# Optimization experiments

Hardware: AMD Instinct MI355X
Metric: run time of the kernel (lower is better)

The kernel has to match this reference:

```python
import jax, jax.numpy as jnp
import numpy as np

B, S, E = 32, 720, 862
PRED_LEN = S
FREQ_TOPK = 20
WINDOW = 24  # fixed optimal_window (code fallback/default candidate)
EPS_VAR = 1e-5


def _main_freq_part(x, k):
    # x: [B, S, E]; rfft over time axis
    xf = jnp.fft.rfft(x, axis=1)                      # [B, F, E] complex
    F = xf.shape[1]
    mag = jnp.moveaxis(jnp.abs(xf), 1, 2)             # [B, E, F]
    _, idx = jax.lax.top_k(mag, k)                    # [B, E, k]
    mask = jnp.sum(jax.nn.one_hot(idx, F, dtype=x.dtype), axis=2)  # [B, E, F]
    mask = jnp.moveaxis(mask, 2, 1)                   # [B, F, E]
    x_filtered = jnp.fft.irfft(xf * mask, axis=1).astype(jnp.float32)  # S even -> length S
    return x - x_filtered, x_filtered


def _window_stats(x, w):
    # Sliding-window mean/std (biased var) with replicate padding, via cumsum.
    pad = w // 2
    xp = jnp.pad(x, ((0, 0), (pad, pad), (0, 0)), mode='edge')  # [B, S+w, E]
    z = jnp.zeros_like(xp[:, :1])
    cs = jnp.concatenate([z, jnp.cumsum(xp, axis=1)], axis=1)
    cs2 = jnp.concatenate([z, jnp.cumsum(xp * xp, axis=1)], axis=1)
    s = x.shape[1]
    s1 = cs[:, w:w + s] - cs[:, :s]
    s2 = cs2[:, w:w + s] - cs2[:, :s]
    mean = s1 / w
    var = jnp.maximum(s2 / w - mean * mean, 0.0)
    std = jnp.sqrt(var + EPS_VAR)
    return mean, std


def _mlp_freq(main_freq_T, x_T, Wf1, bf1, Wf2, bf2, Wf3, bf3):
    # main_freq_T, x_T: [B, E, S]
    h = jax.nn.relu(main_freq_T @ Wf1 + bf1)          # [B, E, 64]
    inp = jnp.concatenate([h, x_T], axis=-1)          # [B, E, 64+S]
    h2 = jax.nn.relu(inp @ Wf2 + bf2)                 # [B, E, 128]
    return h2 @ Wf3 + bf3                             # [B, E, pred_len]


def _mlp_pred(stat_T, x_T, Wp1, bp1, Wp2, bp2, Wp3, bp3):
    h = jax.nn.relu(stat_T @ Wp1 + bp1)               # [B, E, 256]
    inp = jnp.concatenate([h, x_T], axis=-1)          # [B, E, 256+S]
    h2 = jax.nn.relu(inp @ Wp2 + bp2)                 # [B, E, 512]
    return h2 @ Wp3 + bp3                             # [B, E, pred_len]


def setup_inputs() -> dict:
    key = jax.random.key(0)
    ks = jax.random.split(key, 13)
    sc = 0.02
    inp = {
        'batch_x': jax.random.normal(ks[0], (B, S, E), dtype=jnp.float32),
        'Wf1': jax.random.normal(ks[1], (S, 64), dtype=jnp.float32) * sc,
        'bf1': jnp.zeros((64,), jnp.float32),
        'Wf2': jax.random.normal(ks[2], (64 + S, 128), dtype=jnp.float32) * sc,
        'bf2': jnp.zeros((128,), jnp.float32),
        'Wf3': jax.random.normal(ks[3], (128, PRED_LEN), dtype=jnp.float32) * sc,
        'bf3': jnp.zeros((PRED_LEN,), jnp.float32),
        'Wp1': jax.random.normal(ks[4], (S, 256), dtype=jnp.float32) * sc,
        'bp1': jnp.zeros((256,), jnp.float32),
        'Wp2': jax.random.normal(ks[5], (256 + S, 512), dtype=jnp.float32) * sc,
        'bp2': jnp.zeros((512,), jnp.float32),
        'Wp3': jax.random.normal(ks[6], (512, PRED_LEN), dtype=jnp.float32) * sc,
        'bp3': jnp.zeros((PRED_LEN,), jnp.float32),
    }
    return inp


def reference(batch_x, Wf1, bf1, Wf2, bf2, Wf3, bf3, Wp1, bp1, Wp2, bp2, Wp3, bp3):
    # DualAN.forward(batch_x, mode='n') with optimal_window fixed to 24.
    norm_input, x_filtered = _main_freq_part(batch_x, FREQ_TOPK)
    x_T = jnp.swapaxes(batch_x, 1, 2)                 # [B, E, S]
    pred_main = jnp.swapaxes(
        _mlp_freq(jnp.swapaxes(x_filtered, 1, 2), x_T, Wf1, bf1, Wf2, bf2, Wf3, bf3), 1, 2)
    mean, std = _window_stats(norm_input, WINDOW)     # [B, S, E]
    norm = (norm_input - mean) / std
    pred_means = jnp.swapaxes(
        _mlp_pred(jnp.swapaxes(mean, 1, 2), x_T, Wp1, bp1, Wp2, bp2, Wp3, bp3), 1, 2)
    pred_stds = jnp.swapaxes(
        _mlp_pred(jnp.swapaxes(std, 1, 2), x_T, Wp1, bp1, Wp2, bp2, Wp3, bp3), 1, 2)
    # forward returns norm; side products (stored as attrs in torch) concatenated
    # along channels so all compute is captured: [B, S, 4*E]
    return jnp.concatenate([norm, pred_main, pred_means, pred_stds], axis=-1)
```

## Files before the change

kernel.cpp:

```cpp
#include <hip/hip_runtime.h>

using short8 = __attribute__((ext_vector_type(8))) short;
using f32x4v = __attribute__((ext_vector_type(4))) float;

constexpr int SS = 720;
constexpr int EE = 862;
constexpr int FF = 361;
constexpr int MR = 27584;
constexpr int NDFT = 724;
constexpr int OUTSTRIDE = 4 * EE;
constexpr double PI2 = 6.283185307179586476925286766559;

__device__ __forceinline__ unsigned short f2bf(float v) {
  unsigned u = __float_as_uint(v);
  u += 0x7fff + ((u >> 16) & 1);
  return (unsigned short)(u >> 16);
}
__device__ __forceinline__ float bf2f(unsigned short h) {
  return __uint_as_float(((unsigned)h) << 16);
}

__global__ __launch_bounds__(256) void build_trig_k(float* __restrict__ W,
                                                    float2* __restrict__ ptab) {
  int t = blockIdx.x;
  int tid = threadIdx.x;
  for (int f = tid; f < NDFT; f += 256) {
    double v = 0.0;
    if (f < FF) {
      int idx = (int)(((long long)f * t) % SS);
      v = cos(PI2 * idx / (double)SS);
    } else if (f < 2 * FF) {
      int ff = f - FF;
      int idx = (int)(((long long)ff * t) % SS);
      v = -sin(PI2 * idx / (double)SS);
    }
    W[(size_t)t * NDFT + f] = (float)v;
  }
  if (tid == 0) {
    double ang = PI2 * t / (double)SS;
    ptab[t] = make_float2((float)cos(ang), (float)sin(ang));
  }
}

__global__ __launch_bounds__(256) void transpose_in_k(const float* __restrict__ x,
                                                      float* __restrict__ xT) {
  __shared__ float tile[32][33];
  int b = blockIdx.z;
  int s0 = blockIdx.x * 32;
  int e0 = blockIdx.y * 32;
  int tx = threadIdx.x, ty = threadIdx.y;
#pragma unroll
  for (int j = 0; j < 4; ++j) {
    int s = s0 + ty + j * 8;
    int e = e0 + tx;
    if (s < SS && e < EE) tile[ty + j * 8][tx] = x[((size_t)b * SS + s) * EE + e];
  }
  __syncthreads();
#pragma unroll
  for (int j = 0; j < 4; ++j) {
    int e = e0 + ty + j * 8;
    int s = s0 + tx;
    if (e < EE && s < SS) xT[((size_t)b * EE + e) * SS + s] = tile[tx][ty + j * 8];
  }
}

__global__ __launch_bounds__(256) void transpose_norm_k(const float* __restrict__ normT,
                                                        float* __restrict__ out) {
  __shared__ float tile[32][33];
  int b = blockIdx.z;
  int e0 = blockIdx.x * 32;
  int s0 = blockIdx.y * 32;
  int tx = threadIdx.x, ty = threadIdx.y;
#pragma unroll
  for (int j = 0; j < 4; ++j) {
    int e = e0 + ty + j * 8;
    int s = s0 + tx;
    if (e < EE && s < SS) tile[ty + j * 8][tx] = normT[((size_t)b * EE + e) * SS + s];
  }
  __syncthreads();
#pragma unroll
  for (int j = 0; j < 4; ++j) {
    int s = s0 + ty + j * 8;
    int e = e0 + tx;
    if (s < SS && e < EE) out[((size_t)b * SS + s) * OUTSTRIDE + e] = tile[tx][ty + j * 8];
  }
}

__global__ __launch_bounds__(256) void dft_gemm_k(const float* __restrict__ A,
                                                  const float* __restrict__ W,
                                                  float* __restrict__ C) {
  __shared__ float As[16][68];
  __shared__ float Bs[16][68];
  int tid = threadIdx.x;
  int row0 = blockIdx.x * 64;
  int n0 = blockIdx.y * 64;
  int tx = tid & 15, ty = tid >> 4;
  int lr = tid >> 2;
  int lkc = (tid & 3) * 4;
  int bkk = tid >> 4;
  int bn = (tid & 15) * 4;
  float acc[4][4] = {};
  for (int k0 = 0; k0 < SS; k0 += 16) {
    float4 av = *(const float4*)(A + (size_t)(row0 + lr) * SS + k0 + lkc);
    float4 bv = make_float4(0.f, 0.f, 0.f, 0.f);
    if (n0 + bn < NDFT) bv = *(const float4*)(W + (size_t)(k0 + bkk) * NDFT + n0 + bn);
    __syncthreads();
    As[lkc + 0][lr] = av.x;
    As[lkc + 1][lr] = av.y;
    As[lkc + 2][lr] = av.z;
    As[lkc + 3][lr] = av.w;
    *(float4*)&Bs[bkk][bn] = bv;
    __syncthreads();
#pragma unroll
    for (int kk = 0; kk < 16; ++kk) {
      float a4[4], b4[4];
      *(float4*)a4 = *(const float4*)&As[kk][ty * 4];
      *(float4*)b4 = *(const float4*)&Bs[kk][tx * 4];
#pragma unroll
      for (int i = 0; i < 4; ++i)
#pragma unroll
        for (int j = 0; j < 4; ++j) acc[i][j] = fmaf(a4[i], b4[j], acc[i][j]);
    }
  }
  int n = n0 + tx * 4;
  if (n < NDFT) {
#pragma unroll
    for (int i = 0; i < 4; ++i) {
      float v[4];
#pragma unroll
      for (int j = 0; j < 4; ++j) v[j] = acc[i][j];
      *(float4*)(C + (size_t)(row0 + ty * 4 + i) * NDFT + n) = *(float4*)v;
    }
  }
}

__global__ __launch_bounds__(256) void conv_w_k(const float* __restrict__ W, int K, int N,
                                                int Kp, unsigned short* __restrict__ WTh,
                                                unsigned short* __restrict__ WTl) {
  int n = blockIdx.x;
  for (int k = threadIdx.x; k < Kp; k += 256) {
    float v = (n < N && k < K) ? W[(size_t)k * N + n] : 0.f;
    unsigned short h = f2bf(v);
    WTh[(size_t)n * Kp + k] = h;
    WTl[(size_t)n * Kp + k] = f2bf(v - bf2f(h));
  }
}

template <int OUTMODE, bool RELU>
__global__ __launch_bounds__(256, 2) void mfma_gemm_k(
    const float* __restrict__ A1, int sA1, int K1,
    const float* __restrict__ A2, int K2, int ktiles,
    const unsigned short* __restrict__ WTh, const unsigned short* __restrict__ WTl,
    int Kp, const float* __restrict__ bias, int N,
    float* __restrict__ Cout, int ldc, int coloff) {
  __shared__ __align__(16) short smem[24576];
  const int tid = threadIdx.x;
  const int wid = tid >> 6, l = tid & 63;
  const int row0 = blockIdx.x * 128;
  const int n0 = blockIdx.y * 64;
  const int lg = l >> 4, lm = l & 15;

  f32x4v acc[2][4];
  const f32x4v zero4 = {0.f, 0.f, 0.f, 0.f};
#pragma unroll
  for (int i = 0; i < 2; ++i)
#pragma unroll
    for (int j = 0; j < 4; ++j) acc[i][j] = zero4;

  for (int kt = 0; kt < ktiles; ++kt) {
    const int k0 = kt * 64;
    const float* src;
    int str, soff, lim;
    if (k0 < K1) { src = A1; str = sA1; soff = k0; lim = K1; }
    else         { src = A2; str = SS;  soff = k0 - K1; lim = K2; }
    __syncthreads();
#pragma unroll
    for (int p = 0; p < 4; ++p) {
      int gid = p * 256 + tid;
      int rw = gid >> 3, c8 = gid & 7;
      int rowg = row0 + rw;
      if (rowg > MR - 1) rowg = MR - 1;
      int col0 = soff + c8 * 8;
      float4 va = make_float4(0.f, 0.f, 0.f, 0.f), vb = va;
      if (col0 < lim) {
        const float* ap = src + (size_t)rowg * str + col0;
        va = *(const float4*)ap;
        vb = *(const float4*)(ap + 4);
      }
      float vv[8] = {va.x, va.y, va.z, va.w, vb.x, vb.y, vb.z, vb.w};
      short8 hi, lo;
#pragma unroll
      for (int q = 0; q < 8; ++q) {
        unsigned short h = f2bf(vv[q]);
        hi[q] = (short)h;
        lo[q] = (short)f2bf(vv[q] - bf2f(h));
      }
      int slot = rw * 64 + ((c8 ^ (rw & 7)) << 3);
      *(short8*)&smem[slot] = hi;
      *(short8*)&smem[8192 + slot] = lo;
    }
#pragma unroll
    for (int p = 0; p < 2; ++p) {
      int gid = p * 256 + tid;
      int rw = gid >> 3, c8 = gid & 7;
      size_t goff = (size_t)(n0 + rw) * Kp + k0 + c8 * 8;
      short8 vh = *(const short8*)(WTh + goff);
      short8 vl = *(const short8*)(WTl + goff);
      int slot = rw * 64 + ((c8 ^ (rw & 7)) << 3);
      *(short8*)&smem[16384 + slot] = vh;
      *(short8*)&smem[20480 + slot] = vl;
    }
    __syncthreads();
#pragma unroll
    for (int ks = 0; ks < 2; ++ks) {
      short8 ah[2], al[2], bh[4], bl[4];
#pragma unroll
      for (int fi = 0; fi < 2; ++fi) {
        int r = wid * 32 + fi * 16 + lm;
        int slot = r * 64 + (((4 * ks + lg) ^ (r & 7)) << 3);
        ah[fi] = *(const short8*)&smem[slot];
        al[fi] = *(const short8*)&smem[8192 + slot];
      }
#pragma unroll
      for (int fj = 0; fj < 4; ++fj) {
        int r = fj * 16 + lm;
        int slot = r * 64 + (((4 * ks + lg) ^ (r & 7)) << 3);
        bh[fj] = *(const short8*)&smem[16384 + slot];
        bl[fj] = *(const short8*)&smem[20480 + slot];
      }
#pragma unroll
      for (int fi = 0; fi < 2; ++fi)
#pragma unroll
        for (int fj = 0; fj < 4; ++fj) {
          acc[fi][fj] = __builtin_amdgcn_mfma_f32_16x16x32_bf16(ah[fi], bh[fj], acc[fi][fj], 0, 0, 0);
          acc[fi][fj] = __builtin_amdgcn_mfma_f32_16x16x32_bf16(ah[fi], bl[fj], acc[fi][fj], 0, 0, 0);
          acc[fi][fj] = __builtin_amdgcn_mfma_f32_16x16x32_bf16(al[fi], bh[fj], acc[fi][fj], 0, 0, 0);
        }
    }
  }

  if constexpr (OUTMODE == 0) {
#pragma unroll
    for (int fi = 0; fi < 2; ++fi)
#pragma unroll
      for (int fj = 0; fj < 4; ++fj) {
        int col = n0 + fj * 16 + lm;
        float bval = bias[col];
#pragma unroll
        for (int q = 0; q < 4; ++q) {
          int row = row0 + wid * 32 + fi * 16 + lg * 4 + q;
          if (row < MR) {
            float v = acc[fi][fj][q] + bval;
            if (RELU) v = fmaxf(v, 0.f);
            Cout[(size_t)row * ldc + col] = v;
          }
        }
      }
  } else {
    __syncthreads();
    float* Ct = (float*)smem;
#pragma unroll
    for (int fi = 0; fi < 2; ++fi)
#pragma unroll
      for (int fj = 0; fj < 4; ++fj) {
        int cl = fj * 16 + lm;
        int coln = n0 + cl;
        float bval = (coln < N) ? bias[coln] : 0.f;
#pragma unroll
        for (int q = 0; q < 4; ++q) {
          int rl = wid * 32 + fi * 16 + lg * 4 + q;
          Ct[cl * 132 + rl] = acc[fi][fj][q] + bval;
        }
      }
    __syncthreads();
#pragma unroll
    for (int it = 0; it < 32; ++it) {
      int idx = it * 256 + tid;
      int e_l = idx & 127, n_l = idx >> 7;
      int row = row0 + e_l, n = n0 + n_l;
      if (row < MR && n < N) {
        int b = row / EE, e = row - b * EE;
        Cout[((size_t)b * SS + n) * OUTSTRIDE + coloff + e] = Ct[n_l * 132 + e_l];
      }
    }
  }
}

__global__ __launch_bounds__(256) void synth_stats_k(
    const float* __restrict__ dft, const float* __restrict__ xT,
    const float2* __restrict__ ptab, float* __restrict__ xfT,
    float* __restrict__ meanT, float* __restrict__ stdT, float* __restrict__ normT) {
  __shared__ float cosT[SS], sinT[SS];
  __shared__ float nrowS[4][SS];
  __shared__ int selS[4][20];
  __shared__ float creS[4][20], cimS[4][20];

  const int tid = threadIdx.x;
  const int wid = tid >> 6, l = tid & 63;
  const int row = blockIdx.x * 4 + wid;

  for (int i = tid; i < SS; i += 256) {
    float2 p = ptab[i];
    cosT[i] = p.x;
    sinT[i] = p.y;
  }

  const float* dr = dft + (size_t)row * NDFT;
  float re[6], im[6], mg[6];
#pragma unroll
  for (int s = 0; s < 6; ++s) {
    int f = l + 64 * s;
    if (f < FF) {
      re[s] = dr[f];
      im[s] = dr[FF + f];
      mg[s] = re[s] * re[s] + im[s] * im[s];
    } else {
      re[s] = 0.f; im[s] = 0.f; mg[s] = -1e30f;
    }
  }
  __syncthreads();

  for (int k = 0; k < 20; ++k) {
    float bv = -1e29f;
    int bi = 1 << 30;
#pragma unroll
    for (int s = 0; s < 6; ++s) {
      int f = l + 64 * s;
      if (mg[s] > bv) { bv = mg[s]; bi = f; }
    }
#pragma unroll
    for (int off = 32; off >= 1; off >>= 1) {
      float ov = __shfl_xor(bv, off);
      int oi = __shfl_xor(bi, off);
      if (ov > bv || (ov == bv && oi < bi)) { bv = ov; bi = oi; }
    }
    float rw = 0.f, iw = 0.f;
    int lw = bi & 63;
    if (lw == l) {
      int sw = bi >> 6;
#pragma unroll
      for (int s = 0; s < 6; ++s)
        if (s == sw) { rw = re[s]; iw = im[s]; mg[s] = -2e30f; }
    }
    rw = __shfl(rw, lw);
    iw = __shfl(iw, lw);
    if (l == 0) {
      float cf = (bi == 0 || bi == 360) ? (1.f / 720.f) : (2.f / 720.f);
      selS[wid][k] = bi;
      creS[wid][k] = cf * rw;
      cimS[wid][k] = cf * iw;
    }
  }
  __syncthreads();

  const int t0 = 12 * l;
  float xfv[12];
#pragma unroll
  for (int j = 0; j < 12; ++j) xfv[j] = 0.f;
  for (int k = 0; k < 20; ++k) {
    int f = selS[wid][k];
    float cre = creS[wid][k], cim = cimS[wid][k];
    int i0 = (f * t0) % SS;
    float c = cosT[i0], s = sinT[i0];
    float cr = cosT[f], sr = sinT[f];
#pragma unroll
    for (int j = 0; j < 12; ++j) {
      xfv[j] = fmaf(cre, c, xfv[j]);
      xfv[j] = fmaf(-cim, s, xfv[j]);
      float cn = c * cr - s * sr;
      s = s * cr + c * sr;
      c = cn;
    }
  }

  float nr[12];
  if (l < 60) {
    const float* xr = xT + (size_t)row * SS + t0;
    float4 x0 = *(const float4*)(xr);
    float4 x1 = *(const float4*)(xr + 4);
    float4 x2 = *(const float4*)(xr + 8);
    float xv[12] = {x0.x, x0.y, x0.z, x0.w, x1.x, x1.y, x1.z, x1.w, x2.x, x2.y, x2.z, x2.w};
#pragma unroll
    for (int j = 0; j < 12; ++j) nr[j] = xv[j] - xfv[j];
    float* xfp = xfT + (size_t)row * SS + t0;
    *(float4*)(xfp + 0) = make_float4(xfv[0], xfv[1], xfv[2], xfv[3]);
    *(float4*)(xfp + 4) = make_float4(xfv[4], xfv[5], xfv[6], xfv[7]);
    *(float4*)(xfp + 8) = make_float4(xfv[8], xfv[9], xfv[10], xfv[11]);
    float* np = &nrowS[wid][t0];
    *(float4*)(np + 0) = make_float4(nr[0], nr[1], nr[2], nr[3]);
    *(float4*)(np + 4) = make_float4(nr[4], nr[5], nr[6], nr[7]);
    *(float4*)(np + 8) = make_float4(nr[8], nr[9], nr[10], nr[11]);
  }
  __syncthreads();

  if (l < 60) {
    float s1 = 0.f, s2 = 0.f;
#pragma unroll
    for (int d = -12; d < 12; ++d) {
      int u = t0 + d;
      u = u < 0 ? 0 : u;
      float v = nrowS[wid][u];
      s1 += v;
      s2 = fmaf(v, v, s2);
    }
    float mv[12], sv[12], nv[12];
#pragma unroll
    for (int j = 0; j < 12; ++j) {
      int t = t0 + j;
      float mean = s1 * (1.f / 24.f);
      float var = fmaxf(s2 * (1.f / 24.f) - mean * mean, 0.f);
      float sd = sqrtf(var + 1e-5f);
      mv[j] = mean;
      sv[j] = sd;
      nv[j] = (nr[j] - mean) / sd;
      int ua = t + 12; if (ua > SS - 1) ua = SS - 1;
      int ur = t - 12; if (ur < 0) ur = 0;
      float va = nrowS[wid][ua], vr = nrowS[wid][ur];
      s1 += va - vr;
      s2 += va * va - vr * vr;
    }
    float* mp = meanT + (size_t)row * SS + t0;
    float* sp = stdT + (size_t)row * SS + t0;
    float* op = normT + (size_t)row * SS + t0;
    *(float4*)(mp + 0) = make_float4(mv[0], mv[1], mv[2], mv[3]);
    *(float4*)(mp + 4) = make_float4(mv[4], mv[5], mv[6], mv[7]);
    *(float4*)(mp + 8) = make_float4(mv[8], mv[9], mv[10], mv[11]);
    *(float4*)(sp + 0) = make_float4(sv[0], sv[1], sv[2], sv[3]);
    *(float4*)(sp + 4) = make_float4(sv[4], sv[5], sv[6], sv[7]);
    *(float4*)(sp + 8) = make_float4(sv[8], sv[9], sv[10], sv[11]);
    *(float4*)(op + 0) = make_float4(nv[0], nv[1], nv[2], nv[3]);
    *(float4*)(op + 4) = make_float4(nv[4], nv[5], nv[6], nv[7]);
    *(float4*)(op + 8) = make_float4(nv[8], nv[9], nv[10], nv[11]);
  }
}

extern "C" void kernel_launch(void* const* d_in, const int* in_sizes, int n_in,
                              void* d_out, int out_size, void* d_ws, size_t ws_size,
                              hipStream_t stream) {
  const float* x = (const float*)d_in[0];
  const float* Wf1 = (const float*)d_in[1];
  const float* bf1 = (const float*)d_in[2];
  const float* Wf2 = (const float*)d_in[3];
  const float* bf2 = (const float*)d_in[4];
  const float* Wf3 = (const float*)d_in[5];
  const float* bf3 = (const float*)d_in[6];
  const float* Wp1 = (const float*)d_in[7];
  const float* bp1 = (const float*)d_in[8];
  const float* Wp2 = (const float*)d_in[9];
  const float* bp2 = (const float*)d_in[10];
  const float* Wp3 = (const float*)d_in[11];
  const float* bp3 = (const float*)d_in[12];
  float* out = (float*)d_out;
  float* ws = (float*)d_ws;

  constexpr size_t SZ_MT = (size_t)MR * SS;
  float* xT = ws;
  float* xfT = xT + SZ_MT;
  float* meanT = xfT + SZ_MT;
  float* stdT = meanT + SZ_MT;
  float* trig = stdT + SZ_MT;
  float* ptab = trig + (size_t)SS * NDFT;
  float* region = ptab + 1440;
  float* dftb = region;
  float* h1 = region;
  float* h2 = region + (size_t)MR * 64;
  float* hp = region;
  float* hp2 = region + (size_t)MR * 256;
  float* normT = region + (size_t)MR * 768;
  unsigned short* wts = (unsigned short*)normT;
  unsigned short* wf1h = wts;
  unsigned short* wf1l = wf1h + 64 * 768;
  unsigned short* wf2h = wf1l + 64 * 768;
  unsigned short* wf2l = wf2h + 128 * 832;
  unsigned short* wf3h = wf2l + 128 * 832;
  unsigned short* wf3l = wf3h + 768 * 128;
  unsigned short* wp1h = wf3l + 768 * 128;
  unsigned short* wp1l = wp1h + 256 * 768;
  unsigned short* wp2h = wp1l + 256 * 768;
  unsigned short* wp2l = wp2h + 512 * 1024;
  unsigned short* wp3h = wp2l + 512 * 1024;
  unsigned short* wp3l = wp3h + 768 * 512;

  dim3 tb(32, 8);

  build_trig_k<<<SS, 256, 0, stream>>>(trig, (float2*)ptab);
  transpose_in_k<<<dim3(23, 27, 32), tb, 0, stream>>>(x, xT);
  dft_gemm_k<<<dim3(431, 12), 256, 0, stream>>>(xT, trig, dftb);
  synth_stats_k<<<MR / 4, 256, 0, stream>>>(dftb, xT, (const float2*)ptab, xfT, meanT,
                                            stdT, normT);
  transpose_norm_k<<<dim3(27, 23, 32), tb, 0, stream>>>(normT, out);

  conv_w_k<<<64, 256, 0, stream>>>(Wf1, 720, 64, 768, wf1h, wf1l);
  conv_w_k<<<128, 256, 0, stream>>>(Wf2, 784, 128, 832, wf2h, wf2l);
  conv_w_k<<<768, 256, 0, stream>>>(Wf3, 128, 720, 128, wf3h, wf3l);
  conv_w_k<<<256, 256, 0, stream>>>(Wp1, 720, 256, 768, wp1h, wp1l);
  conv_w_k<<<512, 256, 0, stream>>>(Wp2, 976, 512, 1024, wp2h, wp2l);
  conv_w_k<<<768, 256, 0, stream>>>(Wp3, 512, 720, 512, wp3h, wp3l);

  mfma_gemm_k<0, true><<<dim3(216, 1), 256, 0, stream>>>(
      xfT, SS, SS, nullptr, 0, 12, wf1h, wf1l, 768, bf1, 64, h1, 64, 0);
  mfma_gemm_k<0, true><<<dim3(216, 2), 256, 0, stream>>>(
      h1, 64, 64, xT, SS, 13, wf2h, wf2l, 832, bf2, 128, h2, 128, 0);
  mfma_gemm_k<1, false><<<dim3(216, 12), 256, 0, stream>>>(
      h2, 128, 128, nullptr, 0, 2, wf3h, wf3l, 128, bf3, 720, out, 0, EE);

  mfma_gemm_k<0, true><<<dim3(216, 4), 256, 0, stream>>>(
      meanT, SS, SS, nullptr, 0, 12, wp1h, wp1l, 768, bp1, 256, hp, 256, 0);
  mfma_gemm_k<0, true><<<dim3(216, 8), 256, 0, stream>>>(
      hp, 256, 256, xT, SS, 16, wp2h, wp2l, 1024, bp2, 512, hp2, 512, 0);
  mfma_gemm_k<1, false><<<dim3(216, 12), 256, 0, stream>>>(
      hp2, 512, 512, nullptr, 0, 8, wp3h, wp3l, 512, bp3, 720, out, 0, 2 * EE);

  mfma_gemm_k<0, true><<<dim3(216, 4), 256, 0, stream>>>(
      stdT, SS, SS, nullptr, 0, 12, wp1h, wp1l, 768, bp1, 256, hp, 256, 0);
  mfma_gemm_k<0, true><<<dim3(216, 8), 256, 0, stream>>>(
      hp, 256, 256, xT, SS, 16, wp2h, wp2l, 1024, bp2, 512, hp2, 512, 0);
  mfma_gemm_k<1, false><<<dim3(216, 12), 256, 0, stream>>>(
      hp2, 512, 512, nullptr, 0, 8, wp3h, wp3l, 512, bp3, 720, out, 0, 3 * EE);
}
```

Before: 2.137 ms.

## Store intermediates as pre-split bf16 hi/lo pairs and retile DFT GEMM

Every intermediate activation (transposed input, filtered signal, mean, std, hidden layers) is now written as bf16 hi/lo pairs by its producer, so the MFMA GEMMs load ready-made short8 operands and no longer convert fp32 on every tile load. The DFT GEMM reads the original [B,S,E] input directly with strided per-column loads and moves to 128x128 tiles with a 2x2 register sub-block per thread, which raises reuse. The costs are extra conversion work in the producers, strided uncoalesced-ish A loads in the DFT kernel, and a larger workspace layout.

```diff
diff --git a/kernel.cpp b/kernel.cpp
--- a/kernel.cpp
+++ b/kernel.cpp
@@ -43,7 +43,8 @@
 }
 
 __global__ __launch_bounds__(256) void transpose_in_k(const float* __restrict__ x,
-                                                      float* __restrict__ xT) {
+                                                      unsigned short* __restrict__ xTh,
+                                                      unsigned short* __restrict__ xTl) {
   __shared__ float tile[32][33];
   int b = blockIdx.z;
   int s0 = blockIdx.x * 32;
@@ -60,7 +61,13 @@
   for (int j = 0; j < 4; ++j) {
     int e = e0 + ty + j * 8;
     int s = s0 + tx;
-    if (e < EE && s < SS) xT[((size_t)b * EE + e) * SS + s] = tile[tx][ty + j * 8];
+    if (e < EE && s < SS) {
+      float v = tile[tx][ty + j * 8];
+      unsigned short h = f2bf(v);
+      size_t off = (size_t)(b * EE + e) * SS + s;
+      xTh[off] = h;
+      xTl[off] = f2bf(v - bf2f(h));
+    }
   }
 }
 
@@ -86,52 +93,73 @@
   }
 }
 
-__global__ __launch_bounds__(256) void dft_gemm_k(const float* __restrict__ A,
+__global__ __launch_bounds__(256) void dft_gemm_k(const float* __restrict__ x,
                                                   const float* __restrict__ W,
                                                   float* __restrict__ C) {
-  __shared__ float As[16][68];
-  __shared__ float Bs[16][68];
-  int tid = threadIdx.x;
-  int row0 = blockIdx.x * 64;
-  int n0 = blockIdx.y * 64;
-  int tx = tid & 15, ty = tid >> 4;
-  int lr = tid >> 2;
-  int lkc = (tid & 3) * 4;
-  int bkk = tid >> 4;
-  int bn = (tid & 15) * 4;
-  float acc[4][4] = {};
+  __shared__ float As[16][132];
+  __shared__ float Bs[16][132];
+  const int tid = threadIdx.x;
+  const int n0 = blockIdx.x * 128;
+  const int row0 = blockIdx.y * 128;
+  const int tx = tid & 15, ty = tid >> 4;
+  const int rw = tid & 127;
+  const int kcA = tid >> 7;
+  int rowA = row0 + rw;
+  if (rowA > MR - 1) rowA = MR - 1;
+  const int bA = rowA / EE, eA = rowA - bA * EE;
+  const float* xbase = x + (size_t)bA * (SS * EE) + eA;
+  const int nn = (tid & 31) * 4;
+  const int kkB = tid >> 5;
+
+  float acc[2][2][4][4] = {};
+
   for (int k0 = 0; k0 < SS; k0 += 16) {
-    float4 av = *(const float4*)(A + (size_t)(row0 + lr) * SS + k0 + lkc);
-    float4 bv = make_float4(0.f, 0.f, 0.f, 0.f);
-    if (n0 + bn < NDFT) bv = *(const float4*)(W + (size_t)(k0 + bkk) * NDFT + n0 + bn);
     __syncthreads();
-    As[lkc + 0][lr] = av.x;
-    As[lkc + 1][lr] = av.y;
-    As[lkc + 2][lr] = av.z;
-    As[lkc + 3][lr] = av.w;
-    *(float4*)&Bs[bkk][bn] = bv;
+#pragma unroll
+    for (int p = 0; p < 8; ++p) {
+      int kc = kcA + p * 2;
+      As[kc][rw] = xbase[(size_t)(k0 + kc) * EE];
+    }
+#pragma unroll
+    for (int p = 0; p < 2; ++p) {
+      int kk = kkB + p * 8;
+      float4 bv = make_float4(0.f, 0.f, 0.f, 0.f);
+      if (n0 + nn <= 720) bv = *(const float4*)(W + (size_t)(k0 + kk) * NDFT + n0 + nn);
+      *(float4*)&Bs[kk][nn] = bv;
+    }
     __syncthreads();
 #pragma unroll
     for (int kk = 0; kk < 16; ++kk) {
-      float a4[4], b4[4];
-      *(float4*)a4 = *(const float4*)&As[kk][ty * 4];
-      *(float4*)b4 = *(const float4*)&Bs[kk][tx * 4];
-#pragma unroll
-      for (int i = 0; i < 4; ++i)
-#pragma unroll
-        for (int j = 0; j < 4; ++j) acc[i][j] = fmaf(a4[i], b4[j], acc[i][j]);
-    }
-  }
-  int n = n0 + tx * 4;
-  if (n < NDFT) {
+      float a[2][4], b[2][4];
+      *(float4*)a[0] = *(const float4*)&As[kk][ty * 4];
+      *(float4*)a[1] = *(const float4*)&As[kk][64 + ty * 4];
+      *(float4*)b[0] = *(const float4*)&Bs[kk][tx * 4];
+      *(float4*)b[1] = *(const float4*)&Bs[kk][64 + tx * 4];
+#pragma unroll
+      for (int rg = 0; rg < 2; ++rg)
+#pragma unroll
+        for (int cg = 0; cg < 2; ++cg)
+#pragma unroll
+          for (int i = 0; i < 4; ++i)
+#pragma unroll
+            for (int j = 0; j < 4; ++j)
+              acc[rg][cg][i][j] = fmaf(a[rg][i], b[cg][j], acc[rg][cg][i][j]);
+    }
+  }
+
+#pragma unroll
+  for (int rg = 0; rg < 2; ++rg)
 #pragma unroll
     for (int i = 0; i < 4; ++i) {
-      float v[4];
-#pragma unroll
-      for (int j = 0; j < 4; ++j) v[j] = acc[i][j];
-      *(float4*)(C + (size_t)(row0 + ty * 4 + i) * NDFT + n) = *(float4*)v;
-    }
-  }
+      int r = row0 + rg * 64 + ty * 4 + i;
+      if (r < MR) {
+#pragma unroll
+        for (int cg = 0; cg < 2; ++cg) {
+          int c = n0 + cg * 64 + tx * 4;
+          if (c <= 720) *(float4*)(C + (size_t)r * NDFT + c) = *(float4*)&acc[rg][cg][i][0];
+        }
+      }
+    }
 }
 
 __global__ __launch_bounds__(256) void conv_w_k(const float* __restrict__ W, int K, int N,
@@ -148,11 +176,14 @@
 
 template <int OUTMODE, bool RELU>
 __global__ __launch_bounds__(256, 2) void mfma_gemm_k(
-    const float* __restrict__ A1, int sA1, int K1,
-    const float* __restrict__ A2, int K2, int ktiles,
+    const unsigned short* __restrict__ A1h, const unsigned short* __restrict__ A1l,
+    int sA1, int K1,
+    const unsigned short* __restrict__ A2h, const unsigned short* __restrict__ A2l,
+    int ktiles,
     const unsigned short* __restrict__ WTh, const unsigned short* __restrict__ WTl,
     int Kp, const float* __restrict__ bias, int N,
-    float* __restrict__ Cout, int ldc, int coloff) {
+    unsigned short* __restrict__ Ch, unsigned short* __restrict__ Cl, int ldc,
+    float* __restrict__ outF, int coloff) {
   __shared__ __align__(16) short smem[24576];
   const int tid = threadIdx.x;
   const int wid = tid >> 6, l = tid & 63;
@@ -167,12 +198,14 @@
 #pragma unroll
     for (int j = 0; j < 4; ++j) acc[i][j] = zero4;
 
+  const short8 zero8 = {0, 0, 0, 0, 0, 0, 0, 0};
+
   for (int kt = 0; kt < ktiles; ++kt) {
     const int k0 = kt * 64;
-    const float* src;
+    const unsigned short *srcH, *srcL;
     int str, soff, lim;
-    if (k0 < K1) { src = A1; str = sA1; soff = k0; lim = K1; }
-    else         { src = A2; str = SS;  soff = k0 - K1; lim = K2; }
+    if (k0 < K1) { srcH = A1h; srcL = A1l; str = sA1; soff = k0; lim = K1; }
+    else         { srcH = A2h; srcL = A2l; str = SS;  soff = k0 - K1; lim = SS; }
     __syncthreads();
 #pragma unroll
     for (int p = 0; p < 4; ++p) {
@@ -181,31 +214,23 @@
       int rowg = row0 + rw;
       if (rowg > MR - 1) rowg = MR - 1;
       int col0 = soff + c8 * 8;
-      float4 va = make_float4(0.f, 0.f, 0.f, 0.f), vb = va;
+      short8 vh = zero8, vl = zero8;
       if (col0 < lim) {
-        const float* ap = src + (size_t)rowg * str + col0;
-        va = *(const float4*)ap;
-        vb = *(const float4*)(ap + 4);
-      }
-      float vv[8] = {va.x, va.y, va.z, va.w, vb.x, vb.y, vb.z, vb.w};
-      short8 hi, lo;
-#pragma unroll
-      for (int q = 0; q < 8; ++q) {
-        unsigned short h = f2bf(vv[q]);
-        hi[q] = (short)h;
-        lo[q] = (short)f2bf(vv[q] - bf2f(h));
+        size_t off = (size_t)rowg * str + col0;
+        vh = *(const short8*)(srcH + off);
+        vl = *(const short8*)(srcL + off);
       }
       int slot = rw * 64 + ((c8 ^ (rw & 7)) << 3);
-      *(short8*)&smem[slot] = hi;
-      *(short8*)&smem[8192 + slot] = lo;
+      *(short8*)&smem[slot] = vh;
+      *(short8*)&smem[8192 + slot] = vl;
     }
 #pragma unroll
     for (int p = 0; p < 2; ++p) {
       int gid = p * 256 + tid;
       int rw = gid >> 3, c8 = gid & 7;
-      size_t goff = (size_t)(n0 + rw) * Kp + k0 + c8 * 8;
-      short8 vh = *(const short8*)(WTh + goff);
-      short8 vl = *(const short8*)(WTl + goff);
+      size_t off = (size_t)(n0 + rw) * Kp + k0 + c8 * 8;
+      short8 vh = *(const short8*)(WTh + off);
+      short8 vl = *(const short8*)(WTl + off);
       int slot = rw * 64 + ((c8 ^ (rw & 7)) << 3);
       *(short8*)&smem[16384 + slot] = vh;
       *(short8*)&smem[20480 + slot] = vl;
@@ -252,7 +277,9 @@
           if (row < MR) {
             float v = acc[fi][fj][q] + bval;
             if (RELU) v = fmaxf(v, 0.f);
-            Cout[(size_t)row * ldc + col] = v;
+            unsigned short h = f2bf(v);
+            Ch[(size_t)row * ldc + col] = h;
+            Cl[(size_t)row * ldc + col] = f2bf(v - bf2f(h));
           }
         }
       }
@@ -280,16 +307,35 @@
       int row = row0 + e_l, n = n0 + n_l;
       if (row < MR && n < N) {
         int b = row / EE, e = row - b * EE;
-        Cout[((size_t)b * SS + n) * OUTSTRIDE + coloff + e] = Ct[n_l * 132 + e_l];
-      }
-    }
+        outF[((size_t)b * SS + n) * OUTSTRIDE + coloff + e] = Ct[n_l * 132 + e_l];
+      }
+    }
+  }
+}
+
+__device__ __forceinline__ void store_pair12(unsigned short* __restrict__ ph,
+                                             unsigned short* __restrict__ pl,
+                                             const float* v) {
+#pragma unroll
+  for (int g = 0; g < 3; ++g) {
+    ushort4 hh, ll;
+    unsigned short h;
+    h = f2bf(v[g * 4 + 0]); hh.x = h; ll.x = f2bf(v[g * 4 + 0] - bf2f(h));
+    h = f2bf(v[g * 4 + 1]); hh.y = h; ll.y = f2bf(v[g * 4 + 1] - bf2f(h));
+    h = f2bf(v[g * 4 + 2]); hh.z = h; ll.z = f2bf(v[g * 4 + 2] - bf2f(h));
+    h = f2bf(v[g * 4 + 3]); hh.w = h; ll.w = f2bf(v[g * 4 + 3] - bf2f(h));
+    *(ushort4*)(ph + g * 4) = hh;
+    *(ushort4*)(pl + g * 4) = ll;
   }
 }
 
 __global__ __launch_bounds__(256) void synth_stats_k(
-    const float* __restrict__ dft, const float* __restrict__ xT,
-    const float2* __restrict__ ptab, float* __restrict__ xfT,
-    float* __restrict__ meanT, float* __restrict__ stdT, float* __restrict__ normT) {
+    const float* __restrict__ dft, const unsigned short* __restrict__ xTh,
+    const unsigned short* __restrict__ xTl, const float2* __restrict__ ptab,
+    unsigned short* __restrict__ xfh, unsigned short* __restrict__ xfl,
+    unsigned short* __restrict__ mh, unsigned short* __restrict__ ml,
+    unsigned short* __restrict__ sh, unsigned short* __restrict__ sl,
+    float* __restrict__ normT) {
   __shared__ float cosT[SS], sinT[SS];
   __shared__ float nrowS[4][SS];
   __shared__ int selS[4][20];
@@ -375,17 +421,21 @@
 
   float nr[12];
   if (l < 60) {
-    const float* xr = xT + (size_t)row * SS + t0;
-    float4 x0 = *(const float4*)(xr);
-    float4 x1 = *(const float4*)(xr + 4);
-    float4 x2 = *(const float4*)(xr + 8);
-    float xv[12] = {x0.x, x0.y, x0.z, x0.w, x1.x, x1.y, x1.z, x1.w, x2.x, x2.y, x2.z, x2.w};
+    const unsigned short* xhp = xTh + (size_t)row * SS + t0;
+    const unsigned short* xlp = xTl + (size_t)row * SS + t0;
+    float xv[12];
+#pragma unroll
+    for (int g = 0; g < 3; ++g) {
+      ushort4 h4 = *(const ushort4*)(xhp + g * 4);
+      ushort4 l4 = *(const ushort4*)(xlp + g * 4);
+      xv[g * 4 + 0] = bf2f(h4.x) + bf2f(l4.x);
+      xv[g * 4 + 1] = bf2f(h4.y) + bf2f(l4.y);
+      xv[g * 4 + 2] = bf2f(h4.z) + bf2f(l4.z);
+      xv[g * 4 + 3] = bf2f(h4.w) + bf2f(l4.w);
+    }
 #pragma unroll
     for (int j = 0; j < 12; ++j) nr[j] = xv[j] - xfv[j];
-    float* xfp = xfT + (size_t)row * SS + t0;
-    *(float4*)(xfp + 0) = make_float4(xfv[0], xfv[1], xfv[2], xfv[3]);
-    *(float4*)(xfp + 4) = make_float4(xfv[4], xfv[5], xfv[6], xfv[7]);
-    *(float4*)(xfp + 8) = make_float4(xfv[8], xfv[9], xfv[10], xfv[11]);
+    store_pair12(xfh + (size_t)row * SS + t0, xfl + (size_t)row * SS + t0, xfv);
     float* np = &nrowS[wid][t0];
     *(float4*)(np + 0) = make_float4(nr[0], nr[1], nr[2], nr[3]);
     *(float4*)(np + 4) = make_float4(nr[4], nr[5], nr[6], nr[7]);
@@ -419,15 +469,9 @@
       s1 += va - vr;
       s2 += va * va - vr * vr;
     }
-    float* mp = meanT + (size_t)row * SS + t0;
-    float* sp = stdT + (size_t)row * SS + t0;
+    store_pair12(mh + (size_t)row * SS + t0, ml + (size_t)row * SS + t0, mv);
+    store_pair12(sh + (size_t)row * SS + t0, sl + (size_t)row * SS + t0, sv);
     float* op = normT + (size_t)row * SS + t0;
-    *(float4*)(mp + 0) = make_float4(mv[0], mv[1], mv[2], mv[3]);
-    *(float4*)(mp + 4) = make_float4(mv[4], mv[5], mv[6], mv[7]);
-    *(float4*)(mp + 8) = make_float4(mv[8], mv[9], mv[10], mv[11]);
-    *(float4*)(sp + 0) = make_float4(sv[0], sv[1], sv[2], sv[3]);
-    *(float4*)(sp + 4) = make_float4(sv[4], sv[5], sv[6], sv[7]);
-    *(float4*)(sp + 8) = make_float4(sv[8], sv[9], sv[10], sv[11]);
     *(float4*)(op + 0) = make_float4(nv[0], nv[1], nv[2], nv[3]);
     *(float4*)(op + 4) = make_float4(nv[4], nv[5], nv[6], nv[7]);
     *(float4*)(op + 8) = make_float4(nv[8], nv[9], nv[10], nv[11]);
@@ -453,22 +497,28 @@
   float* out = (float*)d_out;
   float* ws = (float*)d_ws;
 
-  constexpr size_t SZ_MT = (size_t)MR * SS;
-  float* xT = ws;
-  float* xfT = xT + SZ_MT;
-  float* meanT = xfT + SZ_MT;
-  float* stdT = meanT + SZ_MT;
-  float* trig = stdT + SZ_MT;
+  constexpr size_t PSF = (size_t)MR * SS / 2;
+  unsigned short* xTh = (unsigned short*)(ws + 0 * PSF);
+  unsigned short* xTl = (unsigned short*)(ws + 1 * PSF);
+  unsigned short* xfh = (unsigned short*)(ws + 2 * PSF);
+  unsigned short* xfl = (unsigned short*)(ws + 3 * PSF);
+  unsigned short* mh  = (unsigned short*)(ws + 4 * PSF);
+  unsigned short* ml  = (unsigned short*)(ws + 5 * PSF);
+  unsigned short* sh  = (unsigned short*)(ws + 6 * PSF);
+  unsigned short* sl  = (unsigned short*)(ws + 7 * PSF);
+  float* dft = ws + 8 * PSF;
+  float* normT = dft + (size_t)MR * NDFT;
+  float* trig = normT + (size_t)MR * SS;
   float* ptab = trig + (size_t)SS * NDFT;
-  float* region = ptab + 1440;
-  float* dftb = region;
-  float* h1 = region;
-  float* h2 = region + (size_t)MR * 64;
-  float* hp = region;
-  float* hp2 = region + (size_t)MR * 256;
-  float* normT = region + (size_t)MR * 768;
-  unsigned short* wts = (unsigned short*)normT;
-  unsigned short* wf1h = wts;
+
+  unsigned short* h1h = (unsigned short*)dft;
+  unsigned short* h1l = h1h + (size_t)MR * 64;
+  unsigned short* h2h = h1l + (size_t)MR * 64;
+  unsigned short* h2l = h2h + (size_t)MR * 128;
+  unsigned short* hph = h2l + (size_t)MR * 128;
+  unsigned short* hpl = hph + (size_t)MR * 256;
+  unsigned short* wq = (unsigned short*)normT;
+  unsigned short* wf1h = wq;
   unsigned short* wf1l = wf1h + 64 * 768;
   unsigned short* wf2h = wf1l + 64 * 768;
   unsigned short* wf2l = wf2h + 128 * 832;
@@ -480,14 +530,16 @@
   unsigned short* wp2l = wp2h + 512 * 1024;
   unsigned short* wp3h = wp2l + 512 * 1024;
   unsigned short* wp3l = wp3h + 768 * 512;
+  unsigned short* hp2h = wp3l + 768 * 512;
+  unsigned short* hp2l = hp2h + (size_t)MR * 512;
 
   dim3 tb(32, 8);
 
   build_trig_k<<<SS, 256, 0, stream>>>(trig, (float2*)ptab);
-  transpose_in_k<<<dim3(23, 27, 32), tb, 0, stream>>>(x, xT);
-  dft_gemm_k<<<dim3(431, 12), 256, 0, stream>>>(xT, trig, dftb);
-  synth_stats_k<<<MR / 4, 256, 0, stream>>>(dftb, xT, (const float2*)ptab, xfT, meanT,
-                                            stdT, normT);
+  transpose_in_k<<<dim3(23, 27, 32), tb, 0, stream>>>(x, xTh, xTl);
+  dft_gemm_k<<<dim3(6, 216), 256, 0, stream>>>(x, trig, dft);
+  synth_stats_k<<<MR / 4, 256, 0, stream>>>(dft, xTh, xTl, (const float2*)ptab,
+                                            xfh, xfl, mh, ml, sh, sl, normT);
   transpose_norm_k<<<dim3(27, 23, 32), tb, 0, stream>>>(normT, out);
 
   conv_w_k<<<64, 256, 0, stream>>>(Wf1, 720, 64, 768, wf1h, wf1l);
@@ -498,23 +550,32 @@
   conv_w_k<<<768, 256, 0, stream>>>(Wp3, 512, 720, 512, wp3h, wp3l);
 
   mfma_gemm_k<0, true><<<dim3(216, 1), 256, 0, stream>>>(
-      xfT, SS, SS, nullptr, 0, 12, wf1h, wf1l, 768, bf1, 64, h1, 64, 0);
+      xfh, xfl, SS, SS, nullptr, nullptr, 12, wf1h, wf1l, 768, bf1, 64,
+      h1h, h1l, 64, nullptr, 0);
   mfma_gemm_k<0, true><<<dim3(216, 2), 256, 0, stream>>>(
-      h1, 64, 64, xT, SS, 13, wf2h, wf2l, 832, bf2, 128, h2, 128, 0);
+      h1h, h1l, 64, 64, xTh, xTl, 13, wf2h, wf2l, 832, bf2, 128,
+      h2h, h2l, 128, nullptr, 0);
   mfma_gemm_k<1, false><<<dim3(216, 12), 256, 0, stream>>>(
-      h2, 128, 128, nullptr, 0, 2, wf3h, wf3l, 128, bf3, 720, out, 0, EE);
+      h2h, h2l, 128, 128, nullptr, nullptr, 2, wf3h, wf3l, 128, bf3, 720,
+      nullptr, nullptr, 0, out, EE);
 
   mfma_gemm_k<0, true><<<dim3(216, 4), 256, 0, stream>>>(
-      meanT, SS, SS, nullptr, 0, 12, wp1h, wp1l, 768, bp1, 256, hp, 256, 0);
+      mh, ml, SS, SS, nullptr, nullptr, 12, wp1h, wp1l, 768, bp1, 256,
+      hph, hpl, 256, nullptr, 0);
   mfma_gemm_k<0, true><<<dim3(216, 8), 256, 0, stream>>>(
-      hp, 256, 256, xT, SS, 16, wp2h, wp2l, 1024, bp2, 512, hp2, 512, 0);
+      hph, hpl, 256, 256, xTh, xTl, 16, wp2h, wp2l, 1024, bp2, 512,
+      hp2h, hp2l, 512, nullptr, 0);
   mfma_gemm_k<1, false><<<dim3(216, 12), 256, 0, stream>>>(
-      hp2, 512, 512, nullptr, 0, 8, wp3h, wp3l, 512, bp3, 720, out, 0, 2 * EE);
+      hp2h, hp2l, 512, 512, nullptr, nullptr, 8, wp3h, wp3l, 512, bp3, 720,
+      nullptr, nullptr, 0, out, 2 * EE);
 
   mfma_gemm_k<0, true><<<dim3(216, 4), 256, 0, stream>>>(
-      stdT, SS, SS, nullptr, 0, 12, wp1h, wp1l, 768, bp1, 256, hp, 256, 0);
+      sh, sl, SS, SS, nullptr, nullptr, 12, wp1h, wp1l, 768, bp1, 256,
+      hph, hpl, 256, nullptr, 0);
   mfma_gemm_k<0, true><<<dim3(216, 8), 256, 0, stream>>>(
-      hp, 256, 256, xT, SS, 16, wp2h, wp2l, 1024, bp2, 512, hp2, 512, 0);
+      hph, hpl, 256, 256, xTh, xTl, 16, wp2h, wp2l, 1024, bp2, 512,
+      hp2h, hp2l, 512, nullptr, 0);
   mfma_gemm_k<1, false><<<dim3(216, 12), 256, 0, stream>>>(
-      hp2, 512, 512, nullptr, 0, 8, wp3h, wp3l, 512, bp3, 720, out, 0, 3 * EE);
-}
+      hp2h, hp2l, 512, 512, nullptr, nullptr, 8, wp3h, wp3l, 512, bp3, 720,
+      nullptr, nullptr, 0, out, 3 * EE);
+}
```

Result: faster. 1.926 ms (-9.9%).
